# Kernel optimization log

Hardware: AMD Instinct MI355X
Metric: run time of the kernel (lower is better)

The kernel has to match this reference:

```python
import jax, jax.numpy as jnp
import numpy as np

NUM_HEADS = 16


def setup_inputs() -> dict:
    key = jax.random.key(0)
    k1, k2, k3 = jax.random.split(key, 3)
    B, N, C = 8, 1024, 1024
    x = jax.random.normal(k1, (B, N, C), dtype=jnp.float32)
    w_qkv = jax.random.normal(k2, (3 * C, C), dtype=jnp.float32) * (C ** -0.5)
    w_proj = jax.random.normal(k3, (C, C), dtype=jnp.float32) * (C ** -0.5)
    b_proj = jnp.zeros((C,), dtype=jnp.float32)
    return {"x": x, "w_qkv": w_qkv, "w_proj": w_proj, "b_proj": b_proj}


def reference(x, w_qkv, w_proj, b_proj):
    B, N, C = x.shape
    H = NUM_HEADS
    d = C // H
    scale = d ** -0.5
    # qkv projection: (B, N, 3C) -> (3, B, H, N, d)
    qkv = jnp.einsum('bnc,oc->bno', x, w_qkv)
    qkv = qkv.reshape(B, N, 3, H, d).transpose(2, 0, 3, 1, 4)
    q, k, v = qkv[0], qkv[1], qkv[2]
    # spatial attention
    attn = jnp.einsum('bhnd,bhmd->bhnm', q, k) * scale
    attn = jax.nn.softmax(attn, axis=-1)
    out = jnp.einsum('bhnm,bhmd->bhnd', attn, v)
    out = out.transpose(0, 2, 1, 3).reshape(B, N, C)
    # output projection
    return jnp.einsum('bnc,oc->bno', out, w_proj) + b_proj
```

## Files before the change

### kernel.cpp

```cpp
#include <hip/hip_runtime.h>
#include <hip/hip_bf16.h>

typedef unsigned short u16;
typedef unsigned int u32;
typedef __bf16 bf16x8 __attribute__((ext_vector_type(8)));
typedef float f32x4 __attribute__((ext_vector_type(4)));

__device__ __forceinline__ u16 f2b(float f) {
    __bf16 h = (__bf16)f;
    return __builtin_bit_cast(u16, h);
}
__device__ __forceinline__ u32 f2b2(float lo, float hi) {
    return (u32)f2b(lo) | ((u32)f2b(hi) << 16);
}
__device__ __forceinline__ f32x4 mfma16(bf16x8 a, bf16x8 b, f32x4 c) {
    return __builtin_amdgcn_mfma_f32_16x16x32_bf16(a, b, c, 0, 0, 0);
}
__device__ __forceinline__ void async16(const u16* gsrc, u16* ldst) {
    __builtin_amdgcn_global_load_lds(
        (const __attribute__((address_space(1))) void*)gsrc,
        (__attribute__((address_space(3))) void*)ldst, 16, 0, 0);
}

__global__ __launch_bounds__(256) void cvt_all(const float* __restrict__ x,
                                               const float* __restrict__ wq,
                                               const float* __restrict__ wp,
                                               u16* __restrict__ xb,
                                               u16* __restrict__ wqb,
                                               u16* __restrict__ wpb) {
    int i = (blockIdx.x * 256 + threadIdx.x) * 4;
    const float* src; u16* dst; int off; float scl;
    if (i < 8388608)       { src = x;  dst = xb;  off = i;            scl = 1.f; }
    else if (i < 9437184)  { src = wq; dst = wqb; off = i - 8388608;  scl = 0.18033688f; }
    else if (i < 11534336) { src = wq; dst = wqb; off = i - 8388608;  scl = 1.f; }
    else                   { src = wp; dst = wpb; off = i - 11534336; scl = 1.f; }
    float4 f = *(const float4*)(src + off);
    ushort4 o;
    o.x = f2b(f.x * scl); o.y = f2b(f.y * scl);
    o.z = f2b(f.z * scl); o.w = f2b(f.w * scl);
    *(ushort4*)(dst + off) = o;
}

template <bool F32OUT>
__device__ __forceinline__ void gemm_core(const u16* __restrict__ A,
                                          const u16* __restrict__ B,
                                          void* __restrict__ Cptr,
                                          const float* __restrict__ bias,
                                          int N, int K, int bm, int bn,
                                          u16* As, u16* Bs) {
    const int tid  = threadIdx.x;
    const int lane = tid & 63, wid = tid >> 6;
    const int quad = lane >> 4, l16 = lane & 15;
    const int wm = (wid >> 1) * 64, wn = (wid & 1) * 64;
    const int srow = tid >> 2;
    const int scol = (tid & 3) * 8;

    const u16* Abase = A + (size_t)(bm * 128) * K + scol;
    const u16* Bbase = B + (size_t)(bn * 128) * K + scol;

    auto stage = [&](int k0, int buf) {
        u16* as = As + buf * 4096;
        u16* bs = Bs + buf * 4096;
        async16(Abase + (size_t)srow * K + k0,        &as[wid * 512]);
        async16(Abase + (size_t)(64 + srow) * K + k0, &as[2048 + wid * 512]);
        async16(Bbase + (size_t)srow * K + k0,        &bs[wid * 512]);
        async16(Bbase + (size_t)(64 + srow) * K + k0, &bs[2048 + wid * 512]);
    };

    f32x4 acc[4][4] = {};
    stage(0, 0);
    const int NT = K >> 5;

    for (int t = 0; t < NT; ++t) {
        const int cur = t & 1;
        __builtin_amdgcn_s_barrier();
        __builtin_amdgcn_sched_barrier(0);
        if (t + 1 < NT) {
            stage((t + 1) << 5, cur ^ 1);
            asm volatile("s_waitcnt vmcnt(4)" ::: "memory");
        } else {
            asm volatile("s_waitcnt vmcnt(0)" ::: "memory");
        }
        __builtin_amdgcn_s_barrier();
        __builtin_amdgcn_sched_barrier(0);

        const u16* as = As + cur * 4096;
        const u16* bs = Bs + cur * 4096;
        bf16x8 af[4], bfr[4];
#pragma unroll
        for (int mt = 0; mt < 4; mt++)
            af[mt] = *(const bf16x8*)&as[(wm + mt * 16 + l16) * 32 + quad * 8];
#pragma unroll
        for (int nt = 0; nt < 4; nt++)
            bfr[nt] = *(const bf16x8*)&bs[(wn + nt * 16 + l16) * 32 + quad * 8];
#pragma unroll
        for (int mt = 0; mt < 4; mt++)
#pragma unroll
            for (int nt = 0; nt < 4; nt++)
                acc[mt][nt] = mfma16(af[mt], bfr[nt], acc[mt][nt]);
    }
#pragma unroll
    for (int mt = 0; mt < 4; mt++) {
#pragma unroll
        for (int nt = 0; nt < 4; nt++) {
            int row = bm * 128 + wm + mt * 16 + quad * 4;
            int col = bn * 128 + wn + nt * 16 + l16;
            float bv = F32OUT ? bias[col] : 0.f;
#pragma unroll
            for (int r = 0; r < 4; r++) {
                if (F32OUT)
                    ((float*)Cptr)[(size_t)(row + r) * N + col] = acc[mt][nt][r] + bv;
                else
                    ((u16*)Cptr)[(size_t)(row + r) * N + col] = f2b(acc[mt][nt][r]);
            }
        }
    }
}

__global__ __launch_bounds__(256) void gemm_qkvt(const u16* __restrict__ xb,
                                                 const u16* __restrict__ wqkvb,
                                                 u16* __restrict__ qkb,
                                                 u16* __restrict__ vTb) {
    __shared__ u16 As[2 * 128 * 32];
    __shared__ u16 Bs[2 * 128 * 32];
    int id = (blockIdx.x & 7) * 192 + (blockIdx.x >> 3);
    if (id < 1024) {
        gemm_core<false>(xb, wqkvb, qkb, nullptr, 2048, 1024, id >> 4, id & 15, As, Bs);
    } else {
        int t = id - 1024;
        gemm_core<false>(wqkvb + (size_t)2048 * 1024, xb, vTb, nullptr,
                         8192, 1024, t >> 6, t & 63, As, Bs);
    }
}

__global__ __launch_bounds__(256) void gemm_proj(const u16* __restrict__ A,
                                                 const u16* __restrict__ B,
                                                 void* __restrict__ C,
                                                 const float* __restrict__ bias) {
    __shared__ u16 As[2 * 128 * 32];
    __shared__ u16 Bs[2 * 128 * 32];
    gemm_core<true>(A, B, C, bias, 1024, 1024, blockIdx.y, blockIdx.x, As, Bs);
}

__global__ __launch_bounds__(256, 4) void attn_kernel(const u16* __restrict__ qk,
                                                      const u16* __restrict__ vT,
                                                      u16* __restrict__ outb) {
    __shared__ u16 Ks[2][64 * 64];
    __shared__ u16 Vt[2][64 * 64];
    __shared__ u16 Ps[4 * 16 * 64];
    const int tid = threadIdx.x, lane = tid & 63, wid = tid >> 6;
    const int quad = lane >> 4, l16 = lane & 15;
    const int qt = blockIdx.x;
    const int bh = blockIdx.y;
    const int b = bh >> 4, h = bh & 15;
    const size_t base = (size_t)b * 1024;
    const int hoff = h * 64;

    const int sr_ = lane >> 3;
    const int sc_ = ((lane & 7) ^ sr_) * 8;
    const int sw = l16 & 7;

    const u16* qptr = qk + (base + qt * 64 + wid * 16 + l16) * 2048 + hoff + quad * 8;
    bf16x8 bq0 = *(const bf16x8*)qptr;
    bf16x8 bq1 = *(const bf16x8*)(qptr + 32);

    auto stageK = [&](int kt, int bs) {
#pragma unroll
        for (int j = 0; j < 2; ++j) {
            int rg = wid * 16 + j * 8;
            async16(qk + (base + kt * 64 + rg + sr_) * 2048 + 1024 + hoff + sc_,
                    &Ks[bs][rg * 64]);
        }
    };
    auto stageV = [&](int kt, int bs) {
#pragma unroll
        for (int j = 0; j < 2; ++j) {
            int rg = wid * 16 + j * 8;
            async16(vT + (size_t)(hoff + rg + sr_) * 8192 + base + kt * 64 + sc_,
                    &Vt[bs][rg * 64]);
        }
    };
    stageK(0, 0);

    f32x4 Oacc[4] = {};
    f32x4 lacc = {};
    bf16x8 vone;
#pragma unroll
    for (int i = 0; i < 8; ++i) vone[i] = (__bf16)1.0f;
    u16* Pw = &Ps[wid * (16 * 64)];
    bf16x8 ap0, ap1;

    for (int u = 0; u < 16; ++u) {
        const int cur = u & 1;
        __builtin_amdgcn_s_barrier();
        __builtin_amdgcn_sched_barrier(0);
        if (u < 15) stageK(u + 1, cur ^ 1);
        stageV(u, cur);
        if (u < 15) asm volatile("s_waitcnt vmcnt(4)" ::: "memory");
        else        asm volatile("s_waitcnt vmcnt(2)" ::: "memory");
        __builtin_amdgcn_s_barrier();
        __builtin_amdgcn_sched_barrier(0);

        f32x4 sacc[4] = {};
#pragma unroll
        for (int nt = 0; nt < 4; nt++) {
            int row = nt * 16 + l16;
            bf16x8 ak0 = *(const bf16x8*)&Ks[cur][row * 64 + ((quad ^ sw) << 3)];
            bf16x8 ak1 = *(const bf16x8*)&Ks[cur][row * 64 + (((4 + quad) ^ sw) << 3)];
            sacc[nt] = mfma16(ak0, bq0, sacc[nt]);
            sacc[nt] = mfma16(ak1, bq1, sacc[nt]);
        }

        if (u) {
            lacc = mfma16(ap0, vone, lacc);
#pragma unroll
            for (int nv = 0; nv < 4; nv++) {
                int row = nv * 16 + l16;
                bf16x8 bv = *(const bf16x8*)&Vt[cur ^ 1][row * 64 + ((quad ^ sw) << 3)];
                Oacc[nv] = mfma16(ap0, bv, Oacc[nv]);
            }
        }
#pragma unroll
        for (int nt = 0; nt < 2; nt++) {
            float p0 = exp2f(sacc[nt][0]);
            float p1 = exp2f(sacc[nt][1]);
            float p2 = exp2f(sacc[nt][2]);
            float p3 = exp2f(sacc[nt][3]);
            uint2 pk; pk.x = f2b2(p0, p1); pk.y = f2b2(p2, p3);
            *(uint2*)&Pw[l16 * 64 + (((nt * 2 + (quad >> 1)) ^ sw) << 3) + ((quad & 1) << 2)] = pk;
        }
        if (u) {
            lacc = mfma16(ap1, vone, lacc);
#pragma unroll
            for (int nv = 0; nv < 4; nv++) {
                int row = nv * 16 + l16;
                bf16x8 bv = *(const bf16x8*)&Vt[cur ^ 1][row * 64 + (((4 + quad) ^ sw) << 3)];
                Oacc[nv] = mfma16(ap1, bv, Oacc[nv]);
            }
        }
#pragma unroll
        for (int nt = 2; nt < 4; nt++) {
            float p0 = exp2f(sacc[nt][0]);
            float p1 = exp2f(sacc[nt][1]);
            float p2 = exp2f(sacc[nt][2]);
            float p3 = exp2f(sacc[nt][3]);
            uint2 pk; pk.x = f2b2(p0, p1); pk.y = f2b2(p2, p3);
            *(uint2*)&Pw[l16 * 64 + (((nt * 2 + (quad >> 1)) ^ sw) << 3) + ((quad & 1) << 2)] = pk;
        }

        asm volatile("s_waitcnt lgkmcnt(0)" ::: "memory");
        __builtin_amdgcn_wave_barrier();
        __builtin_amdgcn_sched_barrier(0);
        ap0 = *(const bf16x8*)&Pw[l16 * 64 + ((quad ^ sw) << 3)];
        ap1 = *(const bf16x8*)&Pw[l16 * 64 + (((4 + quad) ^ sw) << 3)];
    }

    asm volatile("s_waitcnt vmcnt(0)" ::: "memory");
    __builtin_amdgcn_s_barrier();
    __builtin_amdgcn_sched_barrier(0);
    lacc = mfma16(ap0, vone, lacc);
#pragma unroll
    for (int nv = 0; nv < 4; nv++) {
        int row = nv * 16 + l16;
        bf16x8 bv = *(const bf16x8*)&Vt[1][row * 64 + ((quad ^ sw) << 3)];
        Oacc[nv] = mfma16(ap0, bv, Oacc[nv]);
    }
    lacc = mfma16(ap1, vone, lacc);
#pragma unroll
    for (int nv = 0; nv < 4; nv++) {
        int row = nv * 16 + l16;
        bf16x8 bv = *(const bf16x8*)&Vt[1][row * 64 + (((4 + quad) ^ sw) << 3)];
        Oacc[nv] = mfma16(ap1, bv, Oacc[nv]);
    }

    float inv[4];
#pragma unroll
    for (int r = 0; r < 4; r++) inv[r] = 1.f / lacc[r];

#pragma unroll
    for (int nv = 0; nv < 4; nv++)
#pragma unroll
        for (int r = 0; r < 4; r++) {
            int row = qt * 64 + wid * 16 + quad * 4 + r;
            int col = hoff + nv * 16 + l16;
            outb[(base + row) * 1024 + col] = f2b(Oacc[nv][r] * inv[r]);
        }
}

extern "C" void kernel_launch(void* const* d_in, const int* in_sizes, int n_in,
                              void* d_out, int out_size, void* d_ws, size_t ws_size,
                              hipStream_t stream) {
    const float* x      = (const float*)d_in[0];
    const float* w_qkv  = (const float*)d_in[1];
    const float* w_proj = (const float*)d_in[2];
    const float* b_proj = (const float*)d_in[3];

    char* ws = (char*)d_ws;
    u16* xb     = (u16*)(ws);
    u16* wqkvb  = (u16*)(ws + 16777216);
    u16* wprojb = (u16*)(ws + 23068672);
    u16* qkb    = (u16*)(ws + 25165824);
    u16* vTb    = (u16*)(ws + 58720256);
    u16* attnb  = (u16*)(ws + 75497472);

    cvt_all<<<12288, 256, 0, stream>>>(x, w_qkv, w_proj, xb, wqkvb, wprojb);
    gemm_qkvt<<<1536, 256, 0, stream>>>(xb, wqkvb, qkb, vTb);
    attn_kernel<<<dim3(16, 128), 256, 0, stream>>>(qkb, vTb, attnb);
    gemm_proj<<<dim3(8, 64), 256, 0, stream>>>(attnb, wprojb, d_out, b_proj);
}
```

Baseline: 262.7 us.

## Use single-buffered BK=64 GEMM tiles with XOR-swizzled LDS layout

```diff
diff --git a/kernel.cpp b/kernel.cpp
--- a/kernel.cpp
+++ b/kernel.cpp
@@ -52,52 +52,44 @@
     const int lane = tid & 63, wid = tid >> 6;
     const int quad = lane >> 4, l16 = lane & 15;
     const int wm = (wid >> 1) * 64, wn = (wid & 1) * 64;
-    const int srow = tid >> 2;
-    const int scol = (tid & 3) * 8;
-
-    const u16* Abase = A + (size_t)(bm * 128) * K + scol;
-    const u16* Bbase = B + (size_t)(bn * 128) * K + scol;
-
-    auto stage = [&](int k0, int buf) {
-        u16* as = As + buf * 4096;
-        u16* bs = Bs + buf * 4096;
-        async16(Abase + (size_t)srow * K + k0,        &as[wid * 512]);
-        async16(Abase + (size_t)(64 + srow) * K + k0, &as[2048 + wid * 512]);
-        async16(Bbase + (size_t)srow * K + k0,        &bs[wid * 512]);
-        async16(Bbase + (size_t)(64 + srow) * K + k0, &bs[2048 + wid * 512]);
-    };
+    const int swr = l16 & 7;
+
+    const int srow8  = lane >> 3;
+    const int schunk = ((lane & 7) ^ srow8) << 3;
+
+    const u16* Abase = A + (size_t)(bm * 128) * K;
+    const u16* Bbase = B + (size_t)(bn * 128) * K;
 
     f32x4 acc[4][4] = {};
-    stage(0, 0);
-    const int NT = K >> 5;
-
-    for (int t = 0; t < NT; ++t) {
-        const int cur = t & 1;
-        __builtin_amdgcn_s_barrier();
-        __builtin_amdgcn_sched_barrier(0);
-        if (t + 1 < NT) {
-            stage((t + 1) << 5, cur ^ 1);
-            asm volatile("s_waitcnt vmcnt(4)" ::: "memory");
-        } else {
-            asm volatile("s_waitcnt vmcnt(0)" ::: "memory");
-        }
-        __builtin_amdgcn_s_barrier();
-        __builtin_amdgcn_sched_barrier(0);
-
-        const u16* as = As + cur * 4096;
-        const u16* bs = Bs + cur * 4096;
-        bf16x8 af[4], bfr[4];
-#pragma unroll
-        for (int mt = 0; mt < 4; mt++)
-            af[mt] = *(const bf16x8*)&as[(wm + mt * 16 + l16) * 32 + quad * 8];
-#pragma unroll
-        for (int nt = 0; nt < 4; nt++)
-            bfr[nt] = *(const bf16x8*)&bs[(wn + nt * 16 + l16) * 32 + quad * 8];
-#pragma unroll
-        for (int mt = 0; mt < 4; mt++)
-#pragma unroll
-            for (int nt = 0; nt < 4; nt++)
-                acc[mt][nt] = mfma16(af[mt], bfr[nt], acc[mt][nt]);
+
+    for (int k0 = 0; k0 < K; k0 += 64) {
+        __syncthreads();
+#pragma unroll
+        for (int j = 0; j < 4; ++j) {
+            int rg = wid * 32 + j * 8;
+            async16(Abase + (size_t)(rg + srow8) * K + k0 + schunk, &As[rg * 64]);
+            async16(Bbase + (size_t)(rg + srow8) * K + k0 + schunk, &Bs[rg * 64]);
+        }
+        __syncthreads();
+#pragma unroll
+        for (int s = 0; s < 2; ++s) {
+            bf16x8 af[4], bfr[4];
+#pragma unroll
+            for (int mt = 0; mt < 4; mt++) {
+                int r = wm + mt * 16 + l16;
+                af[mt] = *(const bf16x8*)&As[r * 64 + (((s * 4 + quad) ^ swr) << 3)];
+            }
+#pragma unroll
+            for (int nt = 0; nt < 4; nt++) {
+                int r = wn + nt * 16 + l16;
+                bfr[nt] = *(const bf16x8*)&Bs[r * 64 + (((s * 4 + quad) ^ swr) << 3)];
+            }
+#pragma unroll
+            for (int mt = 0; mt < 4; mt++)
+#pragma unroll
+                for (int nt = 0; nt < 4; nt++)
+                    acc[mt][nt] = mfma16(af[mt], bfr[nt], acc[mt][nt]);
+        }
     }
 #pragma unroll
     for (int mt = 0; mt < 4; mt++) {
@@ -121,9 +113,9 @@
                                                  const u16* __restrict__ wqkvb,
                                                  u16* __restrict__ qkb,
                                                  u16* __restrict__ vTb) {
-    __shared__ u16 As[2 * 128 * 32];
-    __shared__ u16 Bs[2 * 128 * 32];
-    int id = (blockIdx.x & 7) * 192 + (blockIdx.x >> 3);
+    __shared__ u16 As[128 * 64];
+    __shared__ u16 Bs[128 * 64];
+    int id = blockIdx.x;
     if (id < 1024) {
         gemm_core<false>(xb, wqkvb, qkb, nullptr, 2048, 1024, id >> 4, id & 15, As, Bs);
     } else {
@@ -137,8 +129,8 @@
                                                  const u16* __restrict__ B,
                                                  void* __restrict__ C,
                                                  const float* __restrict__ bias) {
-    __shared__ u16 As[2 * 128 * 32];
-    __shared__ u16 Bs[2 * 128 * 32];
+    __shared__ u16 As[128 * 64];
+    __shared__ u16 Bs[128 * 64];
     gemm_core<true>(A, B, C, bias, 1024, 1024, blockIdx.y, blockIdx.x, As, Bs);
 }
 
```

After: 245.3 us. -6.6%, faster.
